# Kernel tuning notes

Hardware: AMD Instinct MI355X
Metric: run time of the kernel (lower is better)

Reference implementation:

```python
import jax, jax.numpy as jnp
import numpy as np

NUM_HEADS = 16

def setup_inputs() -> dict:
    key = jax.random.key(0)
    ks = jax.random.split(key, 7)
    B, N, D = 2, 2048, 1024
    x = jax.random.normal(ks[0], (B, N, D), dtype=jnp.float32)
    gamma = jax.random.uniform(ks[1], (B, NUM_HEADS), dtype=jnp.float32)
    dist_matrix = jax.random.uniform(ks[2], (N, N), dtype=jnp.float32)
    W_qkv = jax.random.normal(ks[3], (D, 3 * D), dtype=jnp.float32) * (D ** -0.5)
    b_qkv = jnp.zeros((3 * D,), dtype=jnp.float32)
    W_proj = jax.random.normal(ks[4], (D, D), dtype=jnp.float32) * (D ** -0.5)
    b_proj = jnp.zeros((D,), dtype=jnp.float32)
    return {"x": x, "gamma": gamma, "dist_matrix": dist_matrix,
            "W_qkv": W_qkv, "b_qkv": b_qkv, "W_proj": W_proj, "b_proj": b_proj}

def reference(x, gamma, dist_matrix, W_qkv, b_qkv, W_proj, b_proj):
    B, N, D = x.shape
    H = NUM_HEADS
    hd = D // H
    scale = D ** -0.5  # standard_scale=False -> dim**-0.5
    # qkv projection: [B,N,3D] -> [3,B,H,N,hd]
    qkv = (x @ W_qkv + b_qkv).reshape(B, N, 3, H, hd).transpose(2, 0, 3, 1, 4)
    q, k, v = qkv[0], qkv[1], qkv[2]
    # scores with zoom bias: [B,H,N,N]
    scores = jnp.einsum('bhnd,bhmd->bhnm', q, k) * scale
    scores = scores - gamma[:, :, None, None] * dist_matrix[None, None, :, :]
    attn = jax.nn.softmax(scores, axis=-1)
    out = jnp.einsum('bhnm,bhmd->bhnd', attn, v)  # [B,H,N,hd]
    out = out.transpose(0, 2, 1, 3).reshape(B, N, D)
    return out @ W_proj + b_proj
```

## Files before the change

kernel.cpp:

```cpp
#include <hip/hip_runtime.h>
#include <cstdint>
#include <cstddef>

#define HD 64
#define NH 16
#define BATCH 2
#define SEQ 2048
#define DIM 1024
#define SCALE 0.03125f
#define LOG2E 1.4426950408889634f
#define QSCALE (SCALE * LOG2E)
#define NT (SEQ / 64)

typedef short bf16x8 __attribute__((ext_vector_type(8)));
typedef float f32x4 __attribute__((ext_vector_type(4)));
typedef float f32x16 __attribute__((ext_vector_type(16)));
typedef unsigned u32x4 __attribute__((ext_vector_type(4)));

#define GL16(gp, lp) __builtin_amdgcn_global_load_lds( \
    (const __attribute__((address_space(1))) unsigned int*)(gp), \
    (__attribute__((address_space(3))) unsigned int*)(lp), 16, 0, 0)

static __device__ __forceinline__ unsigned short f2bf(float f) {
  union { float f; unsigned u; } a; a.f = f;
  unsigned r = a.u + 0x7fffu + ((a.u >> 16) & 1u);
  return (unsigned short)(r >> 16);
}

static __device__ __forceinline__ f32x4 zero4() {
  f32x4 z; z[0] = 0.f; z[1] = 0.f; z[2] = 0.f; z[3] = 0.f; return z;
}

__global__ void convert_x(const float* __restrict__ in, unsigned short* __restrict__ out, int n4) {
  int i = blockIdx.x * blockDim.x + threadIdx.x;
  if (i < n4) {
    float4 v = reinterpret_cast<const float4*>(in)[i];
    ushort4 o;
    o.x = f2bf(v.x); o.y = f2bf(v.y); o.z = f2bf(v.z); o.w = f2bf(v.w);
    reinterpret_cast<ushort4*>(out)[i] = o;
  }
}

__global__ void transpose_convert(const float* __restrict__ in, unsigned short* __restrict__ out,
                                  int R, int C) {
  __shared__ float tile[32][33];
  int bx = blockIdx.x * 32;
  int by = blockIdx.y * 32;
  int tx = threadIdx.x, ty = threadIdx.y;
  #pragma unroll
  for (int i = 0; i < 32; i += 8)
    tile[ty + i][tx] = in[(size_t)(by + ty + i) * C + bx + tx];
  __syncthreads();
  #pragma unroll
  for (int i = 0; i < 32; i += 8)
    out[(size_t)(bx + ty + i) * R + by + tx] = f2bf(tile[tx][ty + i]);
}

__global__ __launch_bounds__(256) void gemm128(
    const unsigned short* __restrict__ A, const unsigned short* __restrict__ Bt,
    const float* __restrict__ bias, int K, int mode,
    unsigned short* __restrict__ qo, unsigned short* __restrict__ ko,
    unsigned short* __restrict__ vo, float* __restrict__ outf) {
  __shared__ __attribute__((aligned(16))) unsigned short As[128 * 64];
  __shared__ __attribute__((aligned(16))) unsigned short Bs[128 * 64];
  const int tid = threadIdx.x;
  const int lane = tid & 63, w = tid >> 6;
  const int lo = lane & 15, hi = lane >> 4;
  const int wm = w >> 1, wn = w & 1;
  const int gx = gridDim.x;
  const int nwg = gx * gridDim.y;
  const int flat = blockIdx.y * gx + blockIdx.x;
  const int swz = (flat & 7) * (nwg >> 3) + (flat >> 3);
  const int m0 = (swz / gx) * 128, n0 = (swz % gx) * 128;
  const int srow = tid >> 3, scol = (tid & 7) * 8;
  const unsigned short* abase = A + (size_t)(m0 + srow) * K + scol;
  const unsigned short* bbase = Bt + (size_t)(n0 + srow) * K + scol;

  f32x4 acc[4][4];
  #pragma unroll
  for (int mr = 0; mr < 4; ++mr)
    #pragma unroll
    for (int nr = 0; nr < 4; ++nr) acc[mr][nr] = zero4();

  const int nkt = K / 64;
  for (int kt = 0; kt < nkt; ++kt) {
    const unsigned short* ak = abase + kt * 64;
    const unsigned short* bk = bbase + kt * 64;
    #pragma unroll
    for (int i = 0; i < 4; ++i) {
      GL16(ak + (size_t)(32 * i) * K, &As[(w * 64 + 256 * i) * 8]);
      GL16(bk + (size_t)(32 * i) * K, &Bs[(w * 64 + 256 * i) * 8]);
    }
    __syncthreads();
    __builtin_amdgcn_s_setprio(1);
    #pragma unroll
    for (int kc = 0; kc < 2; ++kc) {
      bf16x8 af[4], bfr[4];
      #pragma unroll
      for (int mr = 0; mr < 4; ++mr)
        af[mr] = *reinterpret_cast<const bf16x8*>(
            &As[(wm * 64 + mr * 16 + lo) * 64 + kc * 32 + hi * 8]);
      #pragma unroll
      for (int nr = 0; nr < 4; ++nr)
        bfr[nr] = *reinterpret_cast<const bf16x8*>(
            &Bs[(wn * 64 + nr * 16 + lo) * 64 + kc * 32 + hi * 8]);
      #pragma unroll
      for (int mr = 0; mr < 4; ++mr)
        #pragma unroll
        for (int nr = 0; nr < 4; ++nr)
          acc[mr][nr] = __builtin_amdgcn_mfma_f32_16x16x32_bf16(af[mr], bfr[nr], acc[mr][nr], 0, 0, 0);
    }
    __builtin_amdgcn_s_setprio(0);
    __syncthreads();
  }

  #pragma unroll
  for (int nr = 0; nr < 4; ++nr) {
    const int gcol = n0 + wn * 64 + nr * 16 + lo;
    const float bv = bias[gcol];
    #pragma unroll
    for (int mr = 0; mr < 4; ++mr)
      #pragma unroll
      for (int j = 0; j < 4; ++j) {
        const int grow = m0 + wm * 64 + mr * 16 + hi * 4 + j;
        float val = acc[mr][nr][j] + bv;
        if (mode == 0) {
          int which = gcol >> 10;
          int hh = (gcol >> 6) & 15;
          int d = gcol & 63;
          int bb = grow >> 11;
          int n = grow & 2047;
          if (which == 0) {
            qo[((size_t)(bb * NH + hh) * SEQ + n) * HD + d] = f2bf(val * QSCALE);
          } else if (which == 1) {
            ko[((size_t)(bb * NH + hh) * SEQ + n) * HD + d] = f2bf(val);
          } else {
            vo[((size_t)(bb * NH + hh) * HD + d) * SEQ + n] = f2bf(val);
          }
        } else {
          outf[(size_t)grow * DIM + gcol] = val;
        }
      }
  }
}

__global__ __launch_bounds__(256, 2) void attn_kernel(
    const unsigned short* __restrict__ qb, const unsigned short* __restrict__ kb,
    const unsigned short* __restrict__ vtb, const float* __restrict__ gamma,
    const float* __restrict__ dist, unsigned short* __restrict__ ab) {
  __shared__ __attribute__((aligned(16))) unsigned short Ks[2][64 * 64];
  __shared__ __attribute__((aligned(16))) unsigned short Vt[2][64 * 64];
  const int tid = threadIdx.x;
  const int lane = tid & 63;
  const int w = tid >> 6;
  const int q5 = lane & 31;
  const int h5 = lane >> 5;
  const int idx = blockIdx.x;
  const int bh = idx & 31;
  const int qt = idx >> 5;
  const int b = bh >> 4, h = bh & 15;
  const int qrow0 = qt * 128 + w * 32;
  const float g2 = gamma[bh] * LOG2E;

  const size_t base = (size_t)bh * SEQ * HD;
  const size_t vtbase = (size_t)bh * HD * SEQ;

  bf16x8 qf[4];
  #pragma unroll
  for (int ks = 0; ks < 4; ++ks)
    qf[ks] = *reinterpret_cast<const bf16x8*>(
        &qb[base + (size_t)(qrow0 + q5) * HD + ks * 16 + h5 * 8]);

  const float* drow = dist + (size_t)(qrow0 + q5) * SEQ + 4 * h5;

  f32x16 o[2];
  #pragma unroll
  for (int i = 0; i < 16; ++i) { o[0][i] = 0.f; o[1][i] = 0.f; }
  float m_run = -INFINITY;
  float l_run = 0.f;

  const int srow = tid >> 3;
  const int schunk = (tid & 7) ^ (srow & 7);
  const unsigned short* ksrc0 = kb + base + (size_t)srow * HD + schunk * 8;
  const unsigned short* ksrc1 = ksrc0 + (size_t)32 * HD;
  const unsigned short* vsrc0 = vtb + vtbase + (size_t)srow * SEQ + schunk * 8;
  const unsigned short* vsrc1 = vsrc0 + (size_t)32 * SEQ;

  GL16(ksrc0, &Ks[0][w * 512]);
  GL16(ksrc1, &Ks[0][2048 + w * 512]);
  GL16(vsrc0, &Vt[0][w * 512]);
  GL16(vsrc1, &Vt[0][2048 + w * 512]);
  GL16(ksrc0 + (size_t)64 * HD, &Ks[1][w * 512]);
  GL16(ksrc1 + (size_t)64 * HD, &Ks[1][2048 + w * 512]);
  __syncthreads();

  f32x16 sA[2], sB[2];

  #pragma unroll
  for (int i = 0; i < 16; ++i) { sA[0][i] = 0.f; sA[1][i] = 0.f; }
  __builtin_amdgcn_s_setprio(1);
  #pragma unroll
  for (int blk = 0; blk < 2; ++blk)
    #pragma unroll
    for (int ks = 0; ks < 4; ++ks) {
      bf16x8 kf = *reinterpret_cast<const bf16x8*>(
          &Ks[0][(blk * 32 + q5) * 64 + ((ks * 2 + h5) ^ (q5 & 7)) * 8]);
      sA[blk] = __builtin_amdgcn_mfma_f32_32x32x16_bf16(kf, qf[ks], sA[blk], 0, 0, 0);
    }
  __builtin_amdgcn_s_setprio(0);
  __syncthreads();

#define ITER(T, CUR, SCUR, SNXT)                                                       \
  {                                                                                    \
                         \
    f32x4 dv[2][4];                                                                    \
    { const float* dp = drow + (T) * 64;                                               \
      _Pragma("unroll")                                                                \
      for (int blk = 0; blk < 2; ++blk)                                                \
        _Pragma("unroll")                                                              \
        for (int rp = 0; rp < 4; ++rp)                                                 \
          dv[blk][rp] = *reinterpret_cast<const f32x4*>(dp + 32 * blk + 8 * rp);       \
    }                                                                                  \
         \
    if ((T) + 1 < NT) {                                                                \
      _Pragma("unroll")                                                                \
      for (int i = 0; i < 16; ++i) { SNXT[0][i] = 0.f; SNXT[1][i] = 0.f; }             \
      __builtin_amdgcn_s_setprio(1);                                                   \
      _Pragma("unroll")                                                                \
      for (int blk = 0; blk < 2; ++blk)                                                \
        _Pragma("unroll")                                                              \
        for (int ks = 0; ks < 4; ++ks) {                                               \
          bf16x8 kf = *reinterpret_cast<const bf16x8*>(                                \
              &Ks[(CUR) ^ 1][(blk * 32 + q5) * 64 + ((ks * 2 + h5) ^ (q5 & 7)) * 8]);  \
          SNXT[blk] = __builtin_amdgcn_mfma_f32_32x32x16_bf16(kf, qf[ks], SNXT[blk], 0, 0, 0); \
        }                                                                              \
      __builtin_amdgcn_s_setprio(0);                                                   \
    }                                                                                  \
           \
    if ((T) + 2 < NT) {                                                                \
      const size_t m2 = (size_t)((T) + 2) * 64;                                        \
      GL16(ksrc0 + m2 * HD, &Ks[CUR][w * 512]);                                        \
      GL16(ksrc1 + m2 * HD, &Ks[CUR][2048 + w * 512]);                                 \
    }                                                                                  \
    if ((T) + 1 < NT) {                                                                \
      const int m1 = ((T) + 1) * 64;                                                   \
      GL16(vsrc0 + m1, &Vt[(CUR) ^ 1][w * 512]);                                       \
      GL16(vsrc1 + m1, &Vt[(CUR) ^ 1][2048 + w * 512]);                                \
    }                                                                                  \
                           \
    float mx[8];                                                                       \
    _Pragma("unroll")                                                                  \
    for (int blk = 0; blk < 2; ++blk)                                                  \
      _Pragma("unroll")                                                                \
      for (int rp = 0; rp < 4; ++rp) {                                                 \
        float v0 = __builtin_fmaf(-g2, dv[blk][rp][0], SCUR[blk][rp * 4 + 0]);         \
        float v1 = __builtin_fmaf(-g2, dv[blk][rp][1], SCUR[blk][rp * 4 + 1]);         \
        float v2 = __builtin_fmaf(-g2, dv[blk][rp][2], SCUR[blk][rp * 4 + 2]);         \
        float v3 = __builtin_fmaf(-g2, dv[blk][rp][3], SCUR[blk][rp * 4 + 3]);         \
        SCUR[blk][rp * 4 + 0] = v0; SCUR[blk][rp * 4 + 1] = v1;                        \
        SCUR[blk][rp * 4 + 2] = v2; SCUR[blk][rp * 4 + 3] = v3;                        \
        mx[blk * 4 + rp] = fmaxf(fmaxf(v0, v1), fmaxf(v2, v3));                        \
      }                                                                                \
    float pm = fmaxf(fmaxf(fmaxf(mx[0], mx[1]), fmaxf(mx[2], mx[3])),                  \
                     fmaxf(fmaxf(mx[4], mx[5]), fmaxf(mx[6], mx[7])));                 \
    pm = fmaxf(pm, __shfl_xor(pm, 32, 64));                                            \
    if (!__all(pm <= m_run + 8.0f)) {                                                  \
      float mn = fmaxf(m_run, pm);                                                     \
      float corr = exp2f(m_run - mn);                                                  \
      m_run = mn;                                                                      \
      l_run *= corr;                                                                   \
      _Pragma("unroll")                                                                \
      for (int i = 0; i < 16; ++i) { o[0][i] *= corr; o[1][i] *= corr; }               \
    }                                                                                  \
    float psum = 0.f;                                                                  \
    unsigned u[2][4][2];                                                               \
    _Pragma("unroll")                                                                  \
    for (int blk = 0; blk < 2; ++blk)                                                  \
      _Pragma("unroll")                                                                \
      for (int rp = 0; rp < 4; ++rp) {                                                 \
        float p0 = exp2f(SCUR[blk][rp * 4 + 0] - m_run);                               \
        float p1 = exp2f(SCUR[blk][rp * 4 + 1] - m_run);                               \
        float p2 = exp2f(SCUR[blk][rp * 4 + 2] - m_run);                               \
        float p3 = exp2f(SCUR[blk][rp * 4 + 3] - m_run);                               \
        psum += (p0 + p1) + (p2 + p3);                                                 \
        asm("v_cvt_pk_bf16_f32 %0, %1, %2" : "=v"(u[blk][rp][0]) : "v"(p0), "v"(p1));  \
        asm("v_cvt_pk_bf16_f32 %0, %1, %2" : "=v"(u[blk][rp][1]) : "v"(p2), "v"(p3));  \
      }                                                                                \
    psum += __shfl_xor(psum, 32, 64);                                                  \
    l_run += psum;                                                                     \
    unsigned pu[4][4];                                                                 \
    _Pragma("unroll")                                                                  \
    for (int blk = 0; blk < 2; ++blk)                                                  \
      _Pragma("unroll")                                                                \
      for (int jp = 0; jp < 2; ++jp) {                                                 \
        unsigned a0 = u[blk][0][jp], b0 = u[blk][1][jp];                               \
        asm("v_permlane32_swap_b32 %0, %1" : "+v"(a0), "+v"(b0));                      \
        pu[2 * blk][jp] = a0; pu[2 * blk][2 + jp] = b0;                                \
        unsigned a1 = u[blk][2][jp], b1 = u[blk][3][jp];                               \
        asm("v_permlane32_swap_b32 %0, %1" : "+v"(a1), "+v"(b1));                      \
        pu[2 * blk + 1][jp] = a1; pu[2 * blk + 1][2 + jp] = b1;                        \
      }                                                                                \
                                                               \
    __builtin_amdgcn_s_setprio(1);                                                     \
    _Pragma("unroll")                                                                  \
    for (int ks = 0; ks < 4; ++ks) {                                                   \
      u32x4 t_; t_[0] = pu[ks][0]; t_[1] = pu[ks][1]; t_[2] = pu[ks][2]; t_[3] = pu[ks][3]; \
      bf16x8 pf = __builtin_bit_cast(bf16x8, t_);                                      \
      _Pragma("unroll")                                                                \
      for (int db = 0; db < 2; ++db) {                                                 \
        bf16x8 vtf = *reinterpret_cast<const bf16x8*>(                                 \
            &Vt[CUR][(db * 32 + q5) * 64 + ((ks * 2 + h5) ^ (q5 & 7)) * 8]);           \
        o[db] = __builtin_amdgcn_mfma_f32_32x32x16_bf16(vtf, pf, o[db], 0, 0, 0);      \
      }                                                                                \
    }                                                                                  \
    __builtin_amdgcn_s_setprio(0);                                                     \
    __syncthreads();                                                                   \
  }

  for (int mt = 0; mt < NT; mt += 2) {
    ITER(mt, 0, sA, sB)
    ITER(mt + 1, 1, sB, sA)
  }
#undef ITER

  {
    float rl = 1.0f / l_run;
    size_t row = (size_t)b * SEQ + qrow0 + q5;
    unsigned short* obase = ab + row * DIM + h * HD + 4 * h5;
    #pragma unroll
    for (int db = 0; db < 2; ++db)
      #pragma unroll
      for (int rp = 0; rp < 4; ++rp) {
        ushort4 w4;
        w4.x = f2bf(o[db][rp * 4 + 0] * rl);
        w4.y = f2bf(o[db][rp * 4 + 1] * rl);
        w4.z = f2bf(o[db][rp * 4 + 2] * rl);
        w4.w = f2bf(o[db][rp * 4 + 3] * rl);
        *reinterpret_cast<ushort4*>(&obase[db * 32 + 8 * rp]) = w4;
      }
  }
}

extern "C" void kernel_launch(void* const* d_in, const int* in_sizes, int n_in,
                              void* d_out, int out_size, void* d_ws, size_t ws_size,
                              hipStream_t stream) {
  const float* x     = (const float*)d_in[0];
  const float* gamma = (const float*)d_in[1];
  const float* dist  = (const float*)d_in[2];
  const float* Wqkv  = (const float*)d_in[3];
  const float* bqkv  = (const float*)d_in[4];
  const float* Wproj = (const float*)d_in[5];
  const float* bproj = (const float*)d_in[6];
  float* out = (float*)d_out;

  char* ws = (char*)d_ws;
  unsigned short* xb     = (unsigned short*)(ws);
  unsigned short* wqkvt  = (unsigned short*)(ws + 8388608);
  unsigned short* wprojt = (unsigned short*)(ws + 14680064);
  unsigned short* qbuf   = (unsigned short*)(ws + 16777216);
  unsigned short* kbuf   = (unsigned short*)(ws + 25165824);
  unsigned short* vtbuf  = (unsigned short*)(ws + 33554432);
  unsigned short* abuf   = (unsigned short*)(ws + 41943040);

  convert_x<<<4096, 256, 0, stream>>>(x, xb, (BATCH * SEQ * DIM) / 4);
  transpose_convert<<<dim3(96, 32), dim3(32, 8), 0, stream>>>(Wqkv, wqkvt, DIM, 3 * DIM);
  transpose_convert<<<dim3(32, 32), dim3(32, 8), 0, stream>>>(Wproj, wprojt, DIM, DIM);
  gemm128<<<dim3(24, 32), 256, 0, stream>>>(xb, wqkvt, bqkv, DIM, 0, qbuf, kbuf, vtbuf, nullptr);
  attn_kernel<<<(SEQ / 128) * BATCH * NH, 256, 0, stream>>>(qbuf, kbuf, vtbuf, gamma, dist, abuf);
  gemm128<<<dim3(8, 32), 256, 0, stream>>>(abuf, wprojt, bproj, DIM, 1, nullptr, nullptr, nullptr, out);
}
```

Before: 175.2 us.

## Restructure attention loop pipeline with explicit vmcnt waits and split barriers

Drops the software-pipelined QK^T that computed the next tile's scores one iteration ahead. Each iteration now computes its own scores from the current K buffer. K prefetch distance shrinks from two tiles to one. The full __syncthreads is replaced by explicit s_waitcnt vmcnt plus s_barrier at two points, with the V load for the next tile issued just before the PV MFMAs. This cuts register pressure (one score set instead of two) and makes the waits finer-grained, at the cost of less overlap between the QK MFMAs and the softmax work, and it relies on the vmcnt counts matching the outstanding loads exactly.

```diff
diff --git a/kernel.cpp b/kernel.cpp
--- a/kernel.cpp
+++ b/kernel.cpp
@@ -190,29 +190,13 @@
   GL16(ksrc1, &Ks[0][2048 + w * 512]);
   GL16(vsrc0, &Vt[0][w * 512]);
   GL16(vsrc1, &Vt[0][2048 + w * 512]);
-  GL16(ksrc0 + (size_t)64 * HD, &Ks[1][w * 512]);
-  GL16(ksrc1 + (size_t)64 * HD, &Ks[1][2048 + w * 512]);
-  __syncthreads();
-
-  f32x16 sA[2], sB[2];
-
-  #pragma unroll
-  for (int i = 0; i < 16; ++i) { sA[0][i] = 0.f; sA[1][i] = 0.f; }
-  __builtin_amdgcn_s_setprio(1);
-  #pragma unroll
-  for (int blk = 0; blk < 2; ++blk)
-    #pragma unroll
-    for (int ks = 0; ks < 4; ++ks) {
-      bf16x8 kf = *reinterpret_cast<const bf16x8*>(
-          &Ks[0][(blk * 32 + q5) * 64 + ((ks * 2 + h5) ^ (q5 & 7)) * 8]);
-      sA[blk] = __builtin_amdgcn_mfma_f32_32x32x16_bf16(kf, qf[ks], sA[blk], 0, 0, 0);
-    }
-  __builtin_amdgcn_s_setprio(0);
-  __syncthreads();
-
-#define ITER(T, CUR, SCUR, SNXT)                                                       \
+
+#define ITER(T, CUR)                                                                   \
   {                                                                                    \
-                         \
+      \
+    asm volatile("s_waitcnt vmcnt(2)" ::: "memory");                                   \
+    __builtin_amdgcn_s_barrier();                                                      \
+               \
     f32x4 dv[2][4];                                                                    \
     { const float* dp = drow + (T) * 64;                                               \
       _Pragma("unroll")                                                                \
@@ -221,44 +205,38 @@
         for (int rp = 0; rp < 4; ++rp)                                                 \
           dv[blk][rp] = *reinterpret_cast<const f32x4*>(dp + 32 * blk + 8 * rp);       \
     }                                                                                  \
-         \
+      \
     if ((T) + 1 < NT) {                                                                \
-      _Pragma("unroll")                                                                \
-      for (int i = 0; i < 16; ++i) { SNXT[0][i] = 0.f; SNXT[1][i] = 0.f; }             \
-      __builtin_amdgcn_s_setprio(1);                                                   \
-      _Pragma("unroll")                                                                \
-      for (int blk = 0; blk < 2; ++blk)                                                \
-        _Pragma("unroll")                                                              \
-        for (int ks = 0; ks < 4; ++ks) {                                               \
-          bf16x8 kf = *reinterpret_cast<const bf16x8*>(                                \
-              &Ks[(CUR) ^ 1][(blk * 32 + q5) * 64 + ((ks * 2 + h5) ^ (q5 & 7)) * 8]);  \
-          SNXT[blk] = __builtin_amdgcn_mfma_f32_32x32x16_bf16(kf, qf[ks], SNXT[blk], 0, 0, 0); \
-        }                                                                              \
-      __builtin_amdgcn_s_setprio(0);                                                   \
-    }                                                                                  \
-           \
-    if ((T) + 2 < NT) {                                                                \
-      const size_t m2 = (size_t)((T) + 2) * 64;                                        \
-      GL16(ksrc0 + m2 * HD, &Ks[CUR][w * 512]);                                        \
-      GL16(ksrc1 + m2 * HD, &Ks[CUR][2048 + w * 512]);                                 \
-    }                                                                                  \
-    if ((T) + 1 < NT) {                                                                \
-      const int m1 = ((T) + 1) * 64;                                                   \
-      GL16(vsrc0 + m1, &Vt[(CUR) ^ 1][w * 512]);                                       \
-      GL16(vsrc1 + m1, &Vt[(CUR) ^ 1][2048 + w * 512]);                                \
-    }                                                                                  \
-                           \
+      const size_t m1 = (size_t)((T) + 1) * 64;                                        \
+      GL16(ksrc0 + m1 * HD, &Ks[(CUR) ^ 1][w * 512]);                                  \
+      GL16(ksrc1 + m1 * HD, &Ks[(CUR) ^ 1][2048 + w * 512]);                           \
+    }                                                                                  \
+                                                               \
+    f32x16 s[2];                                                                       \
+    _Pragma("unroll")                                                                  \
+    for (int i = 0; i < 16; ++i) { s[0][i] = 0.f; s[1][i] = 0.f; }                     \
+    __builtin_amdgcn_s_setprio(1);                                                     \
+    _Pragma("unroll")                                                                  \
+    for (int blk = 0; blk < 2; ++blk)                                                  \
+      _Pragma("unroll")                                                                \
+      for (int ks = 0; ks < 4; ++ks) {                                                 \
+        bf16x8 kf = *reinterpret_cast<const bf16x8*>(                                  \
+            &Ks[CUR][(blk * 32 + q5) * 64 + ((ks * 2 + h5) ^ (q5 & 7)) * 8]);          \
+        s[blk] = __builtin_amdgcn_mfma_f32_32x32x16_bf16(kf, qf[ks], s[blk], 0, 0, 0); \
+      }                                                                                \
+    __builtin_amdgcn_s_setprio(0);                                                     \
+                                 \
     float mx[8];                                                                       \
     _Pragma("unroll")                                                                  \
     for (int blk = 0; blk < 2; ++blk)                                                  \
       _Pragma("unroll")                                                                \
       for (int rp = 0; rp < 4; ++rp) {                                                 \
-        float v0 = __builtin_fmaf(-g2, dv[blk][rp][0], SCUR[blk][rp * 4 + 0]);         \
-        float v1 = __builtin_fmaf(-g2, dv[blk][rp][1], SCUR[blk][rp * 4 + 1]);         \
-        float v2 = __builtin_fmaf(-g2, dv[blk][rp][2], SCUR[blk][rp * 4 + 2]);         \
-        float v3 = __builtin_fmaf(-g2, dv[blk][rp][3], SCUR[blk][rp * 4 + 3]);         \
-        SCUR[blk][rp * 4 + 0] = v0; SCUR[blk][rp * 4 + 1] = v1;                        \
-        SCUR[blk][rp * 4 + 2] = v2; SCUR[blk][rp * 4 + 3] = v3;                        \
+        float v0 = __builtin_fmaf(-g2, dv[blk][rp][0], s[blk][rp * 4 + 0]);            \
+        float v1 = __builtin_fmaf(-g2, dv[blk][rp][1], s[blk][rp * 4 + 1]);            \
+        float v2 = __builtin_fmaf(-g2, dv[blk][rp][2], s[blk][rp * 4 + 2]);            \
+        float v3 = __builtin_fmaf(-g2, dv[blk][rp][3], s[blk][rp * 4 + 3]);            \
+        s[blk][rp * 4 + 0] = v0; s[blk][rp * 4 + 1] = v1;                              \
+        s[blk][rp * 4 + 2] = v2; s[blk][rp * 4 + 3] = v3;                              \
         mx[blk * 4 + rp] = fmaxf(fmaxf(v0, v1), fmaxf(v2, v3));                        \
       }                                                                                \
     float pm = fmaxf(fmaxf(fmaxf(mx[0], mx[1]), fmaxf(mx[2], mx[3])),                  \
@@ -278,10 +256,10 @@
     for (int blk = 0; blk < 2; ++blk)                                                  \
       _Pragma("unroll")                                                                \
       for (int rp = 0; rp < 4; ++rp) {                                                 \
-        float p0 = exp2f(SCUR[blk][rp * 4 + 0] - m_run);                               \
-        float p1 = exp2f(SCUR[blk][rp * 4 + 1] - m_run);                               \
-        float p2 = exp2f(SCUR[blk][rp * 4 + 2] - m_run);                               \
-        float p3 = exp2f(SCUR[blk][rp * 4 + 3] - m_run);                               \
+        float p0 = exp2f(s[blk][rp * 4 + 0] - m_run);                                  \
+        float p1 = exp2f(s[blk][rp * 4 + 1] - m_run);                                  \
+        float p2 = exp2f(s[blk][rp * 4 + 2] - m_run);                                  \
+        float p3 = exp2f(s[blk][rp * 4 + 3] - m_run);                                  \
         psum += (p0 + p1) + (p2 + p3);                                                 \
         asm("v_cvt_pk_bf16_f32 %0, %1, %2" : "=v"(u[blk][rp][0]) : "v"(p0), "v"(p1));  \
         asm("v_cvt_pk_bf16_f32 %0, %1, %2" : "=v"(u[blk][rp][1]) : "v"(p2), "v"(p3));  \
@@ -300,6 +278,18 @@
         asm("v_permlane32_swap_b32 %0, %1" : "+v"(a1), "+v"(b1));                      \
         pu[2 * blk + 1][jp] = a1; pu[2 * blk + 1][2 + jp] = b1;                        \
       }                                                                                \
+              \
+    if ((T) + 1 < NT)                                                                  \
+      asm volatile("s_waitcnt vmcnt(2)" ::: "memory");                                 \
+    else                                                                               \
+      asm volatile("s_waitcnt vmcnt(0)" ::: "memory");                                 \
+    __builtin_amdgcn_s_barrier();                                                      \
+            \
+    if ((T) + 1 < NT) {                                                                \
+      const int m1 = ((T) + 1) * 64;                                                   \
+      GL16(vsrc0 + m1, &Vt[(CUR) ^ 1][w * 512]);                                       \
+      GL16(vsrc1 + m1, &Vt[(CUR) ^ 1][2048 + w * 512]);                                \
+    }                                                                                  \
                                                                \
     __builtin_amdgcn_s_setprio(1);                                                     \
     _Pragma("unroll")                                                                  \
@@ -314,12 +304,11 @@
       }                                                                                \
     }                                                                                  \
     __builtin_amdgcn_s_setprio(0);                                                     \
-    __syncthreads();                                                                   \
   }
 
   for (int mt = 0; mt < NT; mt += 2) {
-    ITER(mt, 0, sA, sB)
-    ITER(mt + 1, 1, sB, sA)
+    ITER(mt, 0)
+    ITER(mt + 1, 1)
   }
 #undef ITER
 
```

Measured after the change: 167.9 us. 4.2% less time.
